# Kernel tuning notes

Hardware: AMD Instinct MI355X
Metric: run time of the kernel (lower is better)

## Reference

```python
import jax, jax.numpy as jnp
import numpy as np

N_NODES = 50000
N_EDGES = 800000
D = 128
AVG_D_LOG = 2.833  # log(avg_degree + 1)
EPS = 1e-5


def setup_inputs() -> dict:
    key = jax.random.key(0)
    ks = jax.random.split(key, 8)
    h = jax.random.normal(ks[0], (N_NODES, D), dtype=jnp.float32)
    e = jax.random.normal(ks[1], (N_EDGES, D), dtype=jnp.float32)
    snorm_n = jax.random.uniform(ks[2], (N_NODES, 1), dtype=jnp.float32)
    src = jax.random.randint(ks[3], (N_EDGES,), 0, N_NODES)
    dst = jax.random.randint(ks[4], (N_EDGES,), 0, N_NODES)
    W_pre = jax.random.normal(ks[5], (3 * D, D), dtype=jnp.float32) * 0.05
    b_pre = jnp.zeros((D,), dtype=jnp.float32)
    W_post = jax.random.normal(ks[6], (13 * D, D), dtype=jnp.float32) * 0.05
    b_post = jnp.zeros((D,), dtype=jnp.float32)
    return {"h": h, "e": e, "snorm_n": snorm_n, "src": src, "dst": dst,
            "W_pre": W_pre, "b_pre": b_pre, "W_post": W_post, "b_post": b_post}


def _pna_forward(h, e, snorm_n, src, dst, W_pre, b_pre, W_post, b_post):
    N = h.shape[0]
    # pretrans_edges: gather endpoint features + edge features, single Linear (pretrans_layers=1)
    z2 = jnp.concatenate([h[src], h[dst], e], axis=1)           # [E, 3D]
    m = z2 @ W_pre + b_pre                                        # [E, D] per-edge message

    # reduce: multi-aggregator mailbox reduce over dst (ragged neighborhoods)
    deg = jax.ops.segment_sum(jnp.ones((m.shape[0],), m.dtype), dst, num_segments=N)  # [N]
    deg_safe = jnp.maximum(deg, 1.0)[:, None]
    s = jax.ops.segment_sum(m, dst, num_segments=N)
    s2 = jax.ops.segment_sum(m * m, dst, num_segments=N)
    mean = s / deg_safe
    var = jax.nn.relu(s2 / deg_safe - mean * mean)
    std = jnp.sqrt(var + EPS)
    mx = jax.ops.segment_max(m, dst, num_segments=N)
    mn = jax.ops.segment_min(m, dst, num_segments=N)
    has = (deg > 0)[:, None]
    mx = jnp.where(has, mx, 0.0)
    mn = jnp.where(has, mn, 0.0)
    agg = jnp.concatenate([mean, mx, mn, std], axis=1)            # [N, 4D]

    # scalers: identity, amplification, attenuation
    log_d = jnp.log(deg[:, None] + 1.0)
    log_d_safe = jnp.log(deg_safe + 1.0)
    amp = agg * (log_d / AVG_D_LOG)
    att = agg * (AVG_D_LOG / log_d_safe)
    scaled = jnp.concatenate([agg, amp, att], axis=1)             # [N, 12D]
    scaled = jnp.where(has, scaled, 0.0)                          # DGL zero-fills zero-degree nodes

    # posttrans: cat original h, single Linear (posttrans_layers=1), then graph_norm
    h_cat = jnp.concatenate([h, scaled], axis=1)                  # [N, 13D]
    out = h_cat @ W_post + b_post                                 # [N, D]
    out = out * snorm_n                                           # graph_norm; dropout p=0 is identity
    return out


def reference(h, e, snorm_n, src, dst, W_pre, b_pre, W_post, b_post):
    return _pna_forward(h, e, snorm_n, src, dst, W_pre, b_pre, W_post, b_post)
```

## Files before the change

### kernel.cpp

```cpp
#include <hip/hip_runtime.h>
#include <math.h>

#define NNODES 50000
#define NEDGES 800000
#define AVGDLOG 2.833f
#define EPSF 1e-5f

typedef __attribute__((ext_vector_type(8))) short short8;
typedef __attribute__((ext_vector_type(4))) float f32x4;

__device__ __forceinline__ unsigned f2bf(float x) {
    unsigned u = __float_as_uint(x);
    return (u + 0x7FFFu + ((u >> 16) & 1u)) >> 16;
}
__device__ __forceinline__ float bf2f(unsigned lo16) {
    return __uint_as_float(lo16 << 16);
}
__device__ __forceinline__ void up8(uint4 v, float* f) {
    f[0] = bf2f(v.x & 0xffffu); f[1] = bf2f(v.x >> 16);
    f[2] = bf2f(v.y & 0xffffu); f[3] = bf2f(v.y >> 16);
    f[4] = bf2f(v.z & 0xffffu); f[5] = bf2f(v.z >> 16);
    f[6] = bf2f(v.w & 0xffffu); f[7] = bf2f(v.w >> 16);
}
__device__ __forceinline__ uint4 pk8(const float* f) {
    uint4 v;
    v.x = f2bf(f[0]) | (f2bf(f[1]) << 16);
    v.y = f2bf(f[2]) | (f2bf(f[3]) << 16);
    v.z = f2bf(f[4]) | (f2bf(f[5]) << 16);
    v.w = f2bf(f[6]) | (f2bf(f[7]) << 16);
    return v;
}

__global__ void k_zero(unsigned* __restrict__ deg) {
    int i = blockIdx.x * 256 + threadIdx.x;
    if (i < NNODES) deg[i] = 0u;
}
__global__ void k_count(const int* __restrict__ dst, unsigned* __restrict__ deg) {
    int i = blockIdx.x * 256 + threadIdx.x;
    if (i < NEDGES) atomicAdd(&deg[dst[i]], 1u);
}
__global__ __launch_bounds__(1024) void k_scan(const unsigned* __restrict__ deg,
                                               int* __restrict__ base, int* __restrict__ cursor) {
    __shared__ int ps[1024];
    const int t = threadIdx.x;
    const int CH = (NNODES + 1023) / 1024;
    int lo = t * CH, hi = min(lo + CH, NNODES);
    int s = 0;
    for (int i = lo; i < hi; ++i) s += (int)deg[i];
    ps[t] = s;
    __syncthreads();
    for (int off = 1; off < 1024; off <<= 1) {
        int v = (t >= off) ? ps[t - off] : 0;
        __syncthreads();
        ps[t] += v;
        __syncthreads();
    }
    int run = (t > 0) ? ps[t - 1] : 0;
    for (int i = lo; i < hi; ++i) {
        base[i] = run; cursor[i] = run;
        run += (int)deg[i];
    }
    if (t == 1023) base[NNODES] = run;
}
__global__ void k_scatter(const int* __restrict__ dst, const int* __restrict__ src,
                          int* __restrict__ cursor, int* __restrict__ sorted,
                          int* __restrict__ ssrc) {
    int i = blockIdx.x * 256 + threadIdx.x;
    if (i < NEDGES) {
        int d = dst[i];
        int slot = atomicAdd(&cursor[d], 1);
        sorted[slot] = i;
        ssrc[slot] = src[i];
    }
}

__global__ void k_convW(const float* __restrict__ Wpre, const float* __restrict__ Wpost,
                        unsigned short* __restrict__ W3t, unsigned short* __restrict__ W12t,
                        unsigned short* __restrict__ Bhat) {
    int i = blockIdx.x * 256 + threadIdx.x;
    if (i < 128 * 128) {
        int n = i & 127, k = i >> 7;
        W3t[n * 128 + k] = (unsigned short)f2bf(Wpre[(256 + k) * 128 + n]);
    }
    if (i < 256 * 128) {
        int n = i >> 7, k = i & 127;
        float v = (n < 128) ? Wpre[k * 128 + n] : Wpre[(128 + k) * 128 + (n - 128)];
        W12t[n * 128 + k] = (unsigned short)f2bf(v);
    }
    if (i < 640 * 384) {
        int kc = i / (384 * 32);
        int rem = i % (384 * 32);
        int n = rem >> 5, kk = rem & 31;
        int k = kc * 32 + kk, c = n & 127, g = n >> 7;
        float v;
        if (g == 0) v = Wpost[k * 128 + c];
        else if (g == 1) v = (k < 128) ? 0.f : Wpost[(512 + k) * 128 + c];
        else v = (k < 128) ? 0.f : Wpost[(1024 + k) * 128 + c];
        Bhat[i] = (unsigned short)f2bf(v);
    }
}

__global__ __launch_bounds__(256) void k_p12(const float* __restrict__ h,
                                             const unsigned short* __restrict__ W12t,
                                             unsigned short* __restrict__ P1,
                                             unsigned short* __restrict__ P2,
                                             unsigned short* __restrict__ Abuf) {
    __shared__ __align__(16) unsigned short As[64 * 128];
    __shared__ __align__(16) unsigned short Bs[256 * 128];
    const int t = threadIdx.x;
    const size_t row0 = (size_t)blockIdx.x * 64;
#pragma unroll
    for (int j = 0; j < 16; ++j) {
        int idx = t + 256 * j;
        int n = idx >> 4, q = idx & 15;
        uint4 wv = *(const uint4*)(W12t + n * 128 + q * 8);
        *(uint4*)((char*)Bs + n * 256 + ((q * 16) ^ ((n & 7) << 4))) = wv;
    }
#pragma unroll
    for (int j = 0; j < 8; ++j) {
        int idx = t + 256 * j;
        int r = idx >> 5, q = idx & 31;
        size_t row = row0 + r;
        uint2 p = {0u, 0u};
        if (row < NNODES) {
            float4 z = ((const float4*)h)[row * 32 + q];
            p.x = f2bf(z.x) | (f2bf(z.y) << 16);
            p.y = f2bf(z.z) | (f2bf(z.w) << 16);
            *(uint2*)(Abuf + row * 640 + q * 4) = p;
        }
        *(uint2*)((char*)As + r * 256 + ((q * 8) ^ ((r & 7) << 4))) = p;
    }
    __syncthreads();
    const int w = t >> 6, lane = t & 63, lrow = lane & 15, lkb = lane >> 4;
    f32x4 acc[16];
#pragma unroll
    for (int i = 0; i < 16; ++i) acc[i] = (f32x4){0.f, 0.f, 0.f, 0.f};
    const char* Abase = (const char*)As + (w * 16 + lrow) * 256;
    const unsigned aswz = (unsigned)(((w * 16 + lrow) & 7) << 4);
#pragma unroll
    for (int kk = 0; kk < 4; ++kk) {
        int kbyte = (kk * 32 + lkb * 8) * 2;
        short8 af = *(const short8*)(Abase + (kbyte ^ aswz));
#pragma unroll
        for (int nt = 0; nt < 16; ++nt) {
            int n = nt * 16 + lrow;
            short8 bf = *(const short8*)((const char*)Bs + n * 256 + (kbyte ^ ((n & 7) << 4)));
            acc[nt] = __builtin_amdgcn_mfma_f32_16x16x32_bf16(af, bf, acc[nt], 0, 0, 0);
        }
    }
#pragma unroll
    for (int half = 0; half < 2; ++half) {
        __syncthreads();
#pragma unroll
        for (int nt = 0; nt < 8; ++nt) {
            int c = nt * 16 + lrow;
#pragma unroll
            for (int i = 0; i < 4; ++i) {
                int lr = w * 16 + lkb * 4 + i;
                *(unsigned short*)((char*)As + lr * 256 + ((c * 2) ^ ((lr & 7) << 4))) =
                    (unsigned short)f2bf(acc[half * 8 + nt][i]);
            }
        }
        __syncthreads();
        unsigned short* dstP = half ? P2 : P1;
#pragma unroll
        for (int j = 0; j < 4; ++j) {
            int idx = t + 256 * j;
            int r = idx >> 4, q = idx & 15;
            size_t row = row0 + r;
            if (row < NNODES) {
                uint4 v = *(const uint4*)((const char*)As + r * 256 + ((q * 16) ^ ((r & 7) << 4)));
                *(uint4*)(dstP + row * 128 + q * 8) = v;
            }
        }
    }
}

__global__ __launch_bounds__(256) void k_gemm_e(const float* __restrict__ e,
                                                const int* __restrict__ sorted,
                                                const unsigned short* __restrict__ W3t,
                                                const float* __restrict__ bpre,
                                                unsigned short* __restrict__ G) {
    __shared__ __align__(16) unsigned short As[64 * 128];
    __shared__ __align__(16) unsigned short Bs[128 * 128];
    __shared__ int Seid[64];
    const int t = threadIdx.x;
    const size_t row0 = (size_t)blockIdx.x * 64;
    if (t < 64) Seid[t] = sorted[row0 + t];
    __syncthreads();
#pragma unroll
    for (int j = 0; j < 8; ++j) {
        int idx = t + 256 * j;
        int n = idx >> 4, q = idx & 15;
        uint4 wv = *(const uint4*)(W3t + n * 128 + q * 8);
        *(uint4*)((char*)Bs + n * 256 + ((q * 16) ^ ((n & 7) << 4))) = wv;
    }
#pragma unroll
    for (int j = 0; j < 8; ++j) {
        int idx = t + 256 * j;
        int r = idx >> 5, q = idx & 31;
        int eid = Seid[r];
        float4 z = ((const float4*)e)[(size_t)eid * 32 + q];
        uint2 p;
        p.x = f2bf(z.x) | (f2bf(z.y) << 16);
        p.y = f2bf(z.z) | (f2bf(z.w) << 16);
        *(uint2*)((char*)As + r * 256 + ((q * 8) ^ ((r & 7) << 4))) = p;
    }
    __syncthreads();
    const int w = t >> 6, lane = t & 63, lrow = lane & 15, lkb = lane >> 4;
    f32x4 acc[8];
#pragma unroll
    for (int i = 0; i < 8; ++i) acc[i] = (f32x4){0.f, 0.f, 0.f, 0.f};
    const char* Abase = (const char*)As + (w * 16 + lrow) * 256;
    const unsigned aswz = (unsigned)(((w * 16 + lrow) & 7) << 4);
#pragma unroll
    for (int kk = 0; kk < 4; ++kk) {
        int kbyte = (kk * 32 + lkb * 8) * 2;
        short8 af = *(const short8*)(Abase + (kbyte ^ aswz));
#pragma unroll
        for (int nt = 0; nt < 8; ++nt) {
            int n = nt * 16 + lrow;
            short8 bf = *(const short8*)((const char*)Bs + n * 256 + (kbyte ^ ((n & 7) << 4)));
            acc[nt] = __builtin_amdgcn_mfma_f32_16x16x32_bf16(af, bf, acc[nt], 0, 0, 0);
        }
    }
#pragma unroll
    for (int nt = 0; nt < 8; ++nt) {
        int c = nt * 16 + lrow;
        float bp = bpre[c];
#pragma unroll
        for (int i = 0; i < 4; ++i) {
            int lr = w * 16 + lkb * 4 + i;
            *(unsigned short*)((char*)As + lr * 256 + ((c * 2) ^ ((lr & 7) << 4))) =
                (unsigned short)f2bf(acc[nt][i] + bp);
        }
    }
    __syncthreads();
#pragma unroll
    for (int j = 0; j < 4; ++j) {
        int idx = t + 256 * j;
        int r = idx >> 4, q = idx & 15;
        uint4 v = *(const uint4*)((const char*)As + r * 256 + ((q * 16) ^ ((r & 7) << 4)));
        *(uint4*)(G + (row0 + r) * 128 + q * 8) = v;
    }
}

__global__ __launch_bounds__(256) void k_reduce(const unsigned short* __restrict__ G,
                                                const unsigned short* __restrict__ P1,
                                                const unsigned short* __restrict__ P2,
                                                const int* __restrict__ basep,
                                                const int* __restrict__ ssrc,
                                                unsigned short* __restrict__ Abuf) {
    const int t = threadIdx.x;
    const int n = blockIdx.x * 4 + (t >> 6);
    const int lane = t & 63, lq = lane >> 4, lc = lane & 15;
    int b0 = basep[n], b1 = basep[n + 1];
    int dg = b1 - b0;
    float s[8], q2[8], mx[8], mn[8];
#pragma unroll
    for (int j = 0; j < 8; ++j) { s[j] = 0.f; q2[j] = 0.f; mx[j] = -3.4e38f; mn[j] = 3.4e38f; }
    if (dg > 0) {
        float p2f[8];
        up8(*(const uint4*)(P2 + (size_t)n * 128 + lc * 8), p2f);
        for (int sl = b0 + lq; sl < b1; sl += 4) {
            int es = ssrc[sl];
            float gf[8], p1f[8];
            up8(*(const uint4*)(G + (size_t)sl * 128 + lc * 8), gf);
            up8(*(const uint4*)(P1 + (size_t)es * 128 + lc * 8), p1f);
#pragma unroll
            for (int j = 0; j < 8; ++j) {
                float m = gf[j] + p1f[j] + p2f[j];
                s[j] += m; q2[j] += m * m;
                mx[j] = fmaxf(mx[j], m); mn[j] = fminf(mn[j], m);
            }
        }
    }
#pragma unroll
    for (int off = 16; off <= 32; off <<= 1) {
#pragma unroll
        for (int j = 0; j < 8; ++j) {
            s[j] += __shfl_xor(s[j], off);
            q2[j] += __shfl_xor(q2[j], off);
            mx[j] = fmaxf(mx[j], __shfl_xor(mx[j], off));
            mn[j] = fminf(mn[j], __shfl_xor(mn[j], off));
        }
    }
    if (lane < 16) {
        float mean[8], sd[8], X[8], N[8];
        if (dg > 0) {
            float ds = (float)dg;
#pragma unroll
            for (int j = 0; j < 8; ++j) {
                mean[j] = s[j] / ds;
                float v = fmaxf(q2[j] / ds - mean[j] * mean[j], 0.f);
                sd[j] = sqrtf(v + EPSF);
                X[j] = mx[j]; N[j] = mn[j];
            }
        } else {
#pragma unroll
            for (int j = 0; j < 8; ++j) { mean[j] = 0.f; sd[j] = 0.f; X[j] = 0.f; N[j] = 0.f; }
        }
        unsigned short* row = Abuf + (size_t)n * 640 + 128 + lc * 8;
        *(uint4*)(row) = pk8(mean);
        *(uint4*)(row + 128) = pk8(X);
        *(uint4*)(row + 256) = pk8(N);
        *(uint4*)(row + 384) = pk8(sd);
    }
}

__global__ __launch_bounds__(512) void k_gemm_post(const unsigned short* __restrict__ Abuf,
                                                   const unsigned short* __restrict__ Bhat,
                                                   const float* __restrict__ bpost,
                                                   const float* __restrict__ snorm,
                                                   const int* __restrict__ basep,
                                                   float* __restrict__ out) {
    __shared__ __align__(16) unsigned short As[2][128 * 32];
    __shared__ __align__(16) unsigned short Bs[2][384 * 32];
    __shared__ float sAmp[128], sAtt[128], sSn[128], sBp[128];
    const int t = threadIdx.x;
    const size_t row0 = (size_t)blockIdx.x * 128;
    if (t < 128) {
        size_t nn = row0 + t;
        float a = 0.f, b = 0.f, sn = 0.f;
        if (nn < NNODES) {
            int dgi = basep[nn + 1] - basep[nn];
            a = logf((float)dgi + 1.f) * (1.f / AVGDLOG);
            b = AVGDLOG / logf(fmaxf((float)dgi, 1.f) + 1.f);
            sn = snorm[nn];
        }
        sAmp[t] = a; sAtt[t] = b; sSn[t] = sn; sBp[t] = bpost[t];
    }
    const int arow = t >> 2, ak4 = t & 3;
    auto loadA = [&](int kc, uint4& ra) {
        ra = (uint4){0u, 0u, 0u, 0u};
        if (row0 + arow < NNODES)
            ra = *(const uint4*)(Abuf + (row0 + arow) * 640 + kc * 32 + ak4 * 8);
    };
    auto loadB = [&](int kc, uint4* rb) {
#pragma unroll
        for (int j = 0; j < 3; ++j) {
            int idx = t + 512 * j;
            int n = idx >> 2, k4 = idx & 3;
            rb[j] = *(const uint4*)(Bhat + ((size_t)kc * 384 + n) * 32 + k4 * 8);
        }
    };
    auto storeLDS = [&](int buf, const uint4& ra, const uint4* rb) {
        *(uint4*)((char*)As[buf] + arow * 64 + ((ak4 * 16) ^ ((arow & 3) << 4))) = ra;
#pragma unroll
        for (int j = 0; j < 3; ++j) {
            int idx = t + 512 * j;
            int n = idx >> 2, k4 = idx & 3;
            *(uint4*)((char*)Bs[buf] + n * 64 + ((k4 * 16) ^ ((n & 3) << 4))) = rb[j];
        }
    };
    const int w = t >> 6, wm = w & 1, wn = w >> 1;
    const int lane = t & 63, lrow = lane & 15, lkb = lane >> 4;
    f32x4 acc[4][6];
#pragma unroll
    for (int a = 0; a < 4; ++a)
#pragma unroll
        for (int b = 0; b < 6; ++b) acc[a][b] = (f32x4){0.f, 0.f, 0.f, 0.f};

    uint4 ra, rb[3];
    loadA(0, ra); loadB(0, rb);
    storeLDS(0, ra, rb);
    int cur = 0;
    for (int kc = 0; kc < 20; ++kc) {
        if (kc < 19) { loadA(kc + 1, ra); loadB(kc + 1, rb); }
        __syncthreads();
        short8 af[4];
#pragma unroll
        for (int mi = 0; mi < 4; ++mi) {
            int r = wm * 64 + mi * 16 + lrow;
            af[mi] = *(const short8*)((const char*)As[cur] + r * 64 + ((lkb * 16) ^ ((r & 3) << 4)));
        }
        short8 bfv[6];
#pragma unroll
        for (int g = 0; g < 3; ++g)
#pragma unroll
            for (int j = 0; j < 2; ++j) {
                int nn = g * 128 + wn * 32 + j * 16 + lrow;
                bfv[g * 2 + j] = *(const short8*)((const char*)Bs[cur] + nn * 64 + ((lkb * 16) ^ ((nn & 3) << 4)));
            }
#pragma unroll
        for (int mi = 0; mi < 4; ++mi)
#pragma unroll
            for (int f = 0; f < 6; ++f)
                acc[mi][f] = __builtin_amdgcn_mfma_f32_16x16x32_bf16(af[mi], bfv[f], acc[mi][f], 0, 0, 0);
        if (kc < 19) storeLDS(cur ^ 1, ra, rb);
        cur ^= 1;
    }
#pragma unroll
    for (int mi = 0; mi < 4; ++mi)
#pragma unroll
        for (int j = 0; j < 2; ++j)
#pragma unroll
            for (int i = 0; i < 4; ++i) {
                int r = wm * 64 + mi * 16 + lkb * 4 + i;
                size_t grow = row0 + r;
                if (grow < NNODES) {
                    int c = wn * 32 + j * 16 + lrow;
                    float v = acc[mi][j][i] + sAmp[r] * acc[mi][2 + j][i] + sAtt[r] * acc[mi][4 + j][i] + sBp[c];
                    out[grow * 128 + c] = v * sSn[r];
                }
            }
}

extern "C" void kernel_launch(void* const* d_in, const int* in_sizes, int n_in,
                              void* d_out, int out_size, void* d_ws, size_t ws_size,
                              hipStream_t stream) {
    const float* h = (const float*)d_in[0];
    const float* e = (const float*)d_in[1];
    const float* snorm = (const float*)d_in[2];
    const int* src = (const int*)d_in[3];
    const int* dst = (const int*)d_in[4];
    const float* Wpre = (const float*)d_in[5];
    const float* bpre = (const float*)d_in[6];
    const float* Wpost = (const float*)d_in[7];
    const float* bpost = (const float*)d_in[8];
    float* out = (float*)d_out;

    char* p = (char*)d_ws;
    auto alloc = [&](size_t bytes) { char* r = p; p += (bytes + 255) & ~(size_t)255; return r; };
    unsigned short* P1 = (unsigned short*)alloc((size_t)NNODES * 128 * 2);
    unsigned short* P2 = (unsigned short*)alloc((size_t)NNODES * 128 * 2);
    unsigned short* Abuf = (unsigned short*)alloc((size_t)NNODES * 640 * 2);
    unsigned short* G = (unsigned short*)alloc((size_t)NEDGES * 128 * 2);
    unsigned short* W3t = (unsigned short*)alloc(128 * 128 * 2);
    unsigned short* W12t = (unsigned short*)alloc(256 * 128 * 2);
    unsigned short* Bhat = (unsigned short*)alloc((size_t)640 * 384 * 2);
    unsigned* deg = (unsigned*)alloc((size_t)NNODES * 4);
    int* basep = (int*)alloc((size_t)(NNODES + 1) * 4);
    int* cursor = (int*)alloc((size_t)NNODES * 4);
    int* sorted = (int*)alloc((size_t)NEDGES * 4);
    int* ssrc = (int*)alloc((size_t)NEDGES * 4);

    k_zero<<<(NNODES + 255) / 256, 256, 0, stream>>>(deg);
    k_count<<<(NEDGES + 255) / 256, 256, 0, stream>>>(dst, deg);
    k_scan<<<1, 1024, 0, stream>>>(deg, basep, cursor);
    k_scatter<<<(NEDGES + 255) / 256, 256, 0, stream>>>(dst, src, cursor, sorted, ssrc);
    k_convW<<<(640 * 384 + 255) / 256, 256, 0, stream>>>(Wpre, Wpost, W3t, W12t, Bhat);
    k_p12<<<(NNODES + 63) / 64, 256, 0, stream>>>(h, W12t, P1, P2, Abuf);
    k_gemm_e<<<NEDGES / 64, 256, 0, stream>>>(e, sorted, W3t, bpre, G);
    k_reduce<<<NNODES / 4, 256, 0, stream>>>(G, P1, P2, basep, ssrc, Abuf);
    k_gemm_post<<<(NNODES + 127) / 128, 512, 0, stream>>>(Abuf, Bhat, bpost, snorm, basep, out);
}
```

Baseline: 561.8 us.

## Make edge GEMM persistent with double-buffered gathers, vectorize scan, and retune LDS swizzle

The edge GEMM kernel now processes 8 tiles of 64 edges per block. It loads the weight matrix into LDS once per block and double-buffers the gathered edge rows, so the global gather for the next tile overlaps the MFMA work on the current one. The scan kernel reads and writes degree chunks with int4 vector accesses. The post GEMM's LDS XOR swizzle now keys on row>>1 to change its bank-conflict pattern. The price is fewer blocks, which means less parallelism for latency hiding, plus more LDS and registers per block.

```diff
diff --git a/kernel.cpp b/kernel.cpp
--- a/kernel.cpp
+++ b/kernel.cpp
@@ -5,6 +5,7 @@
 #define NEDGES 800000
 #define AVGDLOG 2.833f
 #define EPSF 1e-5f
+#define TPB_E 8
 
 typedef __attribute__((ext_vector_type(8))) short short8;
 typedef __attribute__((ext_vector_type(4))) float f32x4;
@@ -43,10 +44,15 @@
                                                int* __restrict__ base, int* __restrict__ cursor) {
     __shared__ int ps[1024];
     const int t = threadIdx.x;
-    const int CH = (NNODES + 1023) / 1024;
-    int lo = t * CH, hi = min(lo + CH, NNODES);
+    const int lo = t * 52;
     int s = 0;
-    for (int i = lo; i < hi; ++i) s += (int)deg[i];
+    if (lo + 52 <= NNODES) {
+        const int4* dp = (const int4*)(deg + lo);
+#pragma unroll
+        for (int i = 0; i < 13; ++i) { int4 v = dp[i]; s += v.x + v.y + v.z + v.w; }
+    } else {
+        for (int i = lo; i < NNODES; ++i) s += (int)deg[i];
+    }
     ps[t] = s;
     __syncthreads();
     for (int off = 1; off < 1024; off <<= 1) {
@@ -56,9 +62,19 @@
         __syncthreads();
     }
     int run = (t > 0) ? ps[t - 1] : 0;
-    for (int i = lo; i < hi; ++i) {
-        base[i] = run; cursor[i] = run;
-        run += (int)deg[i];
+    if (lo + 52 <= NNODES) {
+        const int4* dp = (const int4*)(deg + lo);
+        int4* bp = (int4*)(base + lo);
+        int4* cp = (int4*)(cursor + lo);
+#pragma unroll
+        for (int i = 0; i < 13; ++i) {
+            int4 v = dp[i]; int4 b;
+            b.x = run; run += v.x; b.y = run; run += v.y;
+            b.z = run; run += v.z; b.w = run; run += v.w;
+            bp[i] = b; cp[i] = b;
+        }
+    } else {
+        for (int i = lo; i < NNODES; ++i) { base[i] = run; cursor[i] = run; run += (int)deg[i]; }
     }
     if (t == 1023) base[NNODES] = run;
 }
@@ -181,67 +197,99 @@
                                                 const unsigned short* __restrict__ W3t,
                                                 const float* __restrict__ bpre,
                                                 unsigned short* __restrict__ G) {
-    __shared__ __align__(16) unsigned short As[64 * 128];
     __shared__ __align__(16) unsigned short Bs[128 * 128];
-    __shared__ int Seid[64];
+    __shared__ __align__(16) unsigned short As[2][64 * 128];
+    __shared__ int Seid[TPB_E * 64];
     const int t = threadIdx.x;
-    const size_t row0 = (size_t)blockIdx.x * 64;
-    if (t < 64) Seid[t] = sorted[row0 + t];
+    const int tile0 = blockIdx.x * TPB_E;
+    const int ntiles = min(TPB_E, 12500 - tile0);
+
+    for (int j = t; j < TPB_E * 64; j += 256) {
+        int slot = tile0 * 64 + j;
+        Seid[j] = (slot < NEDGES) ? sorted[slot] : 0;
+    }
     __syncthreads();
+
+    const int q = t & 31, r5 = t >> 5;
+    auto loadE = [&](int ti, float4* ra) {
+#pragma unroll
+        for (int j = 0; j < 8; ++j) {
+            int r = r5 + 8 * j;
+            int eid = Seid[ti * 64 + r];
+            ra[j] = ((const float4*)e)[(size_t)eid * 32 + q];
+        }
+    };
+    auto storeA = [&](int buf, const float4* ra) {
+#pragma unroll
+        for (int j = 0; j < 8; ++j) {
+            int r = r5 + 8 * j;
+            uint2 pv;
+            pv.x = f2bf(ra[j].x) | (f2bf(ra[j].y) << 16);
+            pv.y = f2bf(ra[j].z) | (f2bf(ra[j].w) << 16);
+            *(uint2*)((char*)As[buf] + r * 256 + ((q * 8) ^ ((r & 7) << 4))) = pv;
+        }
+    };
+
+    float4 ra[8];
+    loadE(0, ra);
 #pragma unroll
     for (int j = 0; j < 8; ++j) {
         int idx = t + 256 * j;
-        int n = idx >> 4, q = idx & 15;
-        uint4 wv = *(const uint4*)(W3t + n * 128 + q * 8);
-        *(uint4*)((char*)Bs + n * 256 + ((q * 16) ^ ((n & 7) << 4))) = wv;
-    }
-#pragma unroll
-    for (int j = 0; j < 8; ++j) {
-        int idx = t + 256 * j;
-        int r = idx >> 5, q = idx & 31;
-        int eid = Seid[r];
-        float4 z = ((const float4*)e)[(size_t)eid * 32 + q];
-        uint2 p;
-        p.x = f2bf(z.x) | (f2bf(z.y) << 16);
-        p.y = f2bf(z.z) | (f2bf(z.w) << 16);
-        *(uint2*)((char*)As + r * 256 + ((q * 8) ^ ((r & 7) << 4))) = p;
-    }
+        int n = idx >> 4, qq = idx & 15;
+        uint4 wv = *(const uint4*)(W3t + n * 128 + qq * 8);
+        *(uint4*)((char*)Bs + n * 256 + ((qq * 16) ^ ((n & 7) << 4))) = wv;
+    }
+    storeA(0, ra);
+    if (ntiles > 1) loadE(1, ra);
     __syncthreads();
+
     const int w = t >> 6, lane = t & 63, lrow = lane & 15, lkb = lane >> 4;
-    f32x4 acc[8];
-#pragma unroll
-    for (int i = 0; i < 8; ++i) acc[i] = (f32x4){0.f, 0.f, 0.f, 0.f};
-    const char* Abase = (const char*)As + (w * 16 + lrow) * 256;
-    const unsigned aswz = (unsigned)(((w * 16 + lrow) & 7) << 4);
-#pragma unroll
-    for (int kk = 0; kk < 4; ++kk) {
-        int kbyte = (kk * 32 + lkb * 8) * 2;
-        short8 af = *(const short8*)(Abase + (kbyte ^ aswz));
+    float bpf[8];
+#pragma unroll
+    for (int nt = 0; nt < 8; ++nt) bpf[nt] = bpre[nt * 16 + lrow];
+
+    for (int ti = 0; ti < ntiles; ++ti) {
+        const int c = ti & 1;
+        f32x4 acc[8];
+#pragma unroll
+        for (int i = 0; i < 8; ++i) acc[i] = (f32x4){0.f, 0.f, 0.f, 0.f};
+        const char* Ab = (const char*)As[c] + (w * 16 + lrow) * 256;
+        const unsigned aswz = (unsigned)(((w * 16 + lrow) & 7) << 4);
+#pragma unroll
+        for (int kk = 0; kk < 4; ++kk) {
+            int kbyte = (kk * 32 + lkb * 8) * 2;
+            short8 af = *(const short8*)(Ab + (kbyte ^ aswz));
+#pragma unroll
+            for (int nt = 0; nt < 8; ++nt) {
+                int n = nt * 16 + lrow;
+                short8 bf = *(const short8*)((const char*)Bs + n * 256 + (kbyte ^ ((n & 7) << 4)));
+                acc[nt] = __builtin_amdgcn_mfma_f32_16x16x32_bf16(af, bf, acc[nt], 0, 0, 0);
+            }
+        }
+        __syncthreads();
 #pragma unroll
         for (int nt = 0; nt < 8; ++nt) {
-            int n = nt * 16 + lrow;
-            short8 bf = *(const short8*)((const char*)Bs + n * 256 + (kbyte ^ ((n & 7) << 4)));
-            acc[nt] = __builtin_amdgcn_mfma_f32_16x16x32_bf16(af, bf, acc[nt], 0, 0, 0);
-        }
-    }
-#pragma unroll
-    for (int nt = 0; nt < 8; ++nt) {
-        int c = nt * 16 + lrow;
-        float bp = bpre[c];
-#pragma unroll
-        for (int i = 0; i < 4; ++i) {
-            int lr = w * 16 + lkb * 4 + i;
-            *(unsigned short*)((char*)As + lr * 256 + ((c * 2) ^ ((lr & 7) << 4))) =
-                (unsigned short)f2bf(acc[nt][i] + bp);
-        }
-    }
-    __syncthreads();
-#pragma unroll
-    for (int j = 0; j < 4; ++j) {
-        int idx = t + 256 * j;
-        int r = idx >> 4, q = idx & 15;
-        uint4 v = *(const uint4*)((const char*)As + r * 256 + ((q * 16) ^ ((r & 7) << 4)));
-        *(uint4*)(G + (row0 + r) * 128 + q * 8) = v;
+            int cc = nt * 16 + lrow;
+#pragma unroll
+            for (int i = 0; i < 4; ++i) {
+                int lr = w * 16 + lkb * 4 + i;
+                *(unsigned short*)((char*)As[c] + lr * 256 + ((cc * 2) ^ ((lr & 7) << 4))) =
+                    (unsigned short)f2bf(acc[nt][i] + bpf[nt]);
+            }
+        }
+        if (ti + 1 < ntiles) {
+            storeA(c ^ 1, ra);
+            if (ti + 2 < ntiles) loadE(ti + 2, ra);
+        }
+        __syncthreads();
+        const size_t row0 = (size_t)(tile0 + ti) * 64;
+#pragma unroll
+        for (int j = 0; j < 4; ++j) {
+            int idx = t + 256 * j;
+            int r = idx >> 4, qq = idx & 15;
+            uint4 v = *(const uint4*)((const char*)As[c] + r * 256 + ((qq * 16) ^ ((r & 7) << 4)));
+            *(uint4*)(G + (row0 + r) * 128 + qq * 8) = v;
+        }
     }
 }
 
@@ -345,12 +393,12 @@
         }
     };
     auto storeLDS = [&](int buf, const uint4& ra, const uint4* rb) {
-        *(uint4*)((char*)As[buf] + arow * 64 + ((ak4 * 16) ^ ((arow & 3) << 4))) = ra;
+        *(uint4*)((char*)As[buf] + arow * 64 + ((ak4 * 16) ^ (((arow >> 1) & 3) << 4))) = ra;
 #pragma unroll
         for (int j = 0; j < 3; ++j) {
             int idx = t + 512 * j;
             int n = idx >> 2, k4 = idx & 3;
-            *(uint4*)((char*)Bs[buf] + n * 64 + ((k4 * 16) ^ ((n & 3) << 4))) = rb[j];
+            *(uint4*)((char*)Bs[buf] + n * 64 + ((k4 * 16) ^ (((n >> 1) & 3) << 4))) = rb[j];
         }
     };
     const int w = t >> 6, wm = w & 1, wn = w >> 1;
@@ -372,7 +420,7 @@
 #pragma unroll
         for (int mi = 0; mi < 4; ++mi) {
             int r = wm * 64 + mi * 16 + lrow;
-            af[mi] = *(const short8*)((const char*)As[cur] + r * 64 + ((lkb * 16) ^ ((r & 3) << 4)));
+            af[mi] = *(const short8*)((const char*)As[cur] + r * 64 + ((lkb * 16) ^ (((r >> 1) & 3) << 4)));
         }
         short8 bfv[6];
 #pragma unroll
@@ -380,7 +428,7 @@
 #pragma unroll
             for (int j = 0; j < 2; ++j) {
                 int nn = g * 128 + wn * 32 + j * 16 + lrow;
-                bfv[g * 2 + j] = *(const short8*)((const char*)Bs[cur] + nn * 64 + ((lkb * 16) ^ ((nn & 3) << 4)));
+                bfv[g * 2 + j] = *(const short8*)((const char*)Bs[cur] + nn * 64 + ((lkb * 16) ^ (((nn >> 1) & 3) << 4)));
             }
 #pragma unroll
         for (int mi = 0; mi < 4; ++mi)
@@ -441,7 +489,7 @@
     k_scatter<<<(NEDGES + 255) / 256, 256, 0, stream>>>(dst, src, cursor, sorted, ssrc);
     k_convW<<<(640 * 384 + 255) / 256, 256, 0, stream>>>(Wpre, Wpost, W3t, W12t, Bhat);
     k_p12<<<(NNODES + 63) / 64, 256, 0, stream>>>(h, W12t, P1, P2, Abuf);
-    k_gemm_e<<<NEDGES / 64, 256, 0, stream>>>(e, sorted, W3t, bpre, G);
+    k_gemm_e<<<(12500 + TPB_E - 1) / TPB_E, 256, 0, stream>>>(e, sorted, W3t, bpre, G);
     k_reduce<<<NNODES / 4, 256, 0, stream>>>(G, P1, P2, basep, ssrc, Abuf);
     k_gemm_post<<<(NNODES + 127) / 128, 512, 0, stream>>>(Abuf, Bhat, bpost, snorm, basep, out);
 }
```

After: 479.3 us. -14.7%, faster.
